# Kernel optimization log

Measured on AMD Instinct MI355X. Metric: run time of the kernel, lower is better.

The kernel has to match this reference:

```python
import jax, jax.numpy as jnp
import numpy as np

N, E = 50000, 800000
FN, FE, D, H = 64, 16, 128, 4


def setup_inputs() -> dict:
    key = jax.random.key(0)
    ks = jax.random.split(key, 16)
    inp = {
        "nodes": jax.random.normal(ks[0], (N, FN), jnp.float32),
        "edges": jax.random.normal(ks[1], (E, FE), jnp.float32),
        "senders": jax.random.randint(ks[2], (E,), 0, N, jnp.int32),
        "receivers": jax.random.randint(ks[3], (E,), 0, N, jnp.int32),
        "avg_multi_head": 0,
        # params (orthogonal init approximated by scaled normal; math identical)
        "W_node": jax.random.normal(ks[4], (FN, D), jnp.float32) / np.sqrt(FN),
        "b_node": jnp.zeros((D,), jnp.float32),
        "W_edge": jax.random.normal(ks[5], (FE, D), jnp.float32) / np.sqrt(FE),
        "b_edge": jnp.zeros((D,), jnp.float32),
        "Wk_s": jax.random.normal(ks[6], (H, D, D), jnp.float32) / np.sqrt(D),
        "bk_s": jnp.zeros((H, D), jnp.float32),
        "Wk_r": jax.random.normal(ks[7], (H, D, D), jnp.float32) / np.sqrt(D),
        "bk_r": jnp.zeros((H, D), jnp.float32),
        "W_out": jax.random.normal(ks[8], (H * D, D), jnp.float32) / np.sqrt(H * D),
        "b_out": jnp.zeros((D,), jnp.float32),
    }
    return inp


def _segment_softmax(logits, seg_ids, num_segments):
    seg_max = jax.ops.segment_max(logits, seg_ids, num_segments=num_segments)
    seg_max = jnp.where(jnp.isfinite(seg_max), seg_max, 0.0)  # empty segments
    e = jnp.exp(logits - seg_max[seg_ids])
    seg_sum = jax.ops.segment_sum(e, seg_ids, num_segments=num_segments)
    return e / seg_sum[seg_ids]


def reference(nodes, edges, senders, receivers, avg_multi_head,
              W_node, b_node, W_edge, b_edge, Wk_s, bk_s, Wk_r, bk_r,
              W_out, b_out):
    n_node = nodes.shape[0]
    x = nodes @ W_node + b_node            # [N, D] projected nodes
    ef = edges @ W_edge + b_edge           # [E, D] projected edge features
    sa = x[senders]                        # [E, D] sent attributes
    ra = x[receivers]                      # [E, D] received attributes
    scale = 1.0 / jnp.sqrt(jnp.asarray(D, x.dtype))
    heads = []
    for h in range(H):  # small fixed head count, structurally distinct params
        k_s = sa @ Wk_s[h] + bk_s[h]                 # [E, D]
        k_r = ra @ Wk_r[h] + bk_r[h] + ef            # [E, D]
        logits = jnp.sum(k_s * k_r, axis=1) * scale  # [E]
        w = _segment_softmax(logits, receivers, n_node)
        msg = w[:, None] * (sa + ef)                 # [E, D]
        heads.append(jax.ops.segment_sum(msg, receivers, num_segments=n_node))
    if avg_multi_head:
        agg = jnp.mean(jnp.stack(heads), axis=0)
    else:
        agg = jnp.concatenate(heads, axis=1) @ W_out + b_out
    return jax.nn.relu(x + agg)            # new node features [N, D]
```

## Files before the change

kernel.cpp:

```cpp
#include <hip/hip_runtime.h>

typedef unsigned short u16;
typedef unsigned int u32;
typedef short bh8 __attribute__((ext_vector_type(8)));
typedef float f4 __attribute__((ext_vector_type(4)));
typedef float pf2 __attribute__((ext_vector_type(2)));

__device__ __forceinline__ float bf2f(u16 h) { return __uint_as_float(((u32)h) << 16); }
__device__ __forceinline__ float bflo(u32 u) { return __uint_as_float(u << 16); }
__device__ __forceinline__ float bfhi(u32 u) { return __uint_as_float(u & 0xffff0000u); }
__device__ __forceinline__ u16 f2bf(float f) {
    u32 x = __float_as_uint(f);
    return (u16)((x + 0x7fffu + ((x >> 16) & 1u)) >> 16);
}
__device__ __forceinline__ pf2 pkfma(pf2 a, pf2 b, pf2 c) {
    pf2 d;
    asm("v_pk_fma_f32 %0, %1, %2, %3" : "=v"(d) : "v"(a), "v"(b), "v"(c));
    return d;
}
__device__ __forceinline__ pf2 u2f2(u32 u) {
    pf2 r;
    r.x = bflo(u);
    r.y = bfhi(u);
    return r;
}
__device__ __forceinline__ float dpp_red16(float x) {
    int y;
    y = __builtin_amdgcn_update_dpp(0, __float_as_int(x), 0xB1, 0xF, 0xF, true);
    x += __int_as_float(y);
    y = __builtin_amdgcn_update_dpp(0, __float_as_int(x), 0x4E, 0xF, 0xF, true);
    x += __int_as_float(y);
    y = __builtin_amdgcn_update_dpp(0, __float_as_int(x), 0x141, 0xF, 0xF, true);
    x += __int_as_float(y);
    y = __builtin_amdgcn_update_dpp(0, __float_as_int(x), 0x140, 0xF, 0xF, true);
    x += __int_as_float(y);
    return x;
}

#define KSCL 0.12751744336457488f

__global__ void k0a_kernel(const float* __restrict__ Wn, const float* __restrict__ Wks,
                           const float* __restrict__ Wkr, const float* __restrict__ Wout,
                           const float* __restrict__ bn, const float* __restrict__ bks,
                           const float* __restrict__ bkr, float* __restrict__ A,
                           float* __restrict__ B, u16* __restrict__ WoT,
                           float* __restrict__ ybs, float* __restrict__ ybr) {
    int idx = blockIdx.x * 256 + threadIdx.x;
    if (idx < 65536) {
        int which = idx >> 15;
        int rem = idx & 32767;
        int h = rem >> 13;
        int r = rem & 8191;
        int a = r >> 7, dp = r & 127;
        const float* W = which ? Wks : Wkr;
        float acc = 0.f;
        for (int d = 0; d < 128; ++d)
            acc += Wn[a * 128 + d] * W[(h * 128 + d) * 128 + dp];
        (which ? B : A)[(h * 64 + a) * 128 + dp] = acc;
    } else if (idx < 131072) {
        int j = idx - 65536;
        int c = j >> 9, k = j & 511;
        WoT[j] = f2bf(Wout[(size_t)k * 128 + c]);
    } else if (idx < 132096) {
        int j = idx - 131072;
        int which = j >> 9;
        int rem = j & 511;
        int h = rem >> 7, dp = rem & 127;
        const float* W = which ? Wks : Wkr;
        const float* b = which ? bks : bkr;
        float acc = b[h * 128 + dp];
        for (int d = 0; d < 128; ++d) acc += bn[d] * W[(h * 128 + d) * 128 + dp];
        (which ? ybs : ybr)[h * 128 + dp] = acc;
    }
}

__global__ void k0b_kernel(const float* __restrict__ Wn, const float* __restrict__ bn,
                           const float* __restrict__ A, const float* __restrict__ B,
                           const float* __restrict__ ybr, const float* __restrict__ ybs,
                           const float* __restrict__ Wks, const float* __restrict__ Wedge,
                           const float* __restrict__ bks, const float* __restrict__ bedge,
                           u16* __restrict__ WfT, float* __restrict__ biasrow) {
    int idx = blockIdx.x * 256 + threadIdx.x;
    if (idx >= 65 * 708 + 60 * 64) return;
    if (idx >= 65 * 708) {
        int j = idx - 65 * 708;
        WfT[(708 + (j >> 6)) * 64 + (j & 63)] = 0;
        return;
    }
    int a = idx / 708, c = idx % 708;
    float val;
    if (c < 128) {
        val = (a < 64) ? Wn[a * 128 + c] : bn[c];
    } else if (c < 640) {
        int h = (c - 128) >> 7, i = (c - 128) & 127;
        const float* rv = (a < 64) ? &A[(h * 64 + a) * 128] : &ybr[h * 128];
        float s = 0.f;
        for (int d = 0; d < 128; ++d) s += rv[d] * Wks[(h * 128 + i) * 128 + d];
        val = s;
    } else if (c < 704) {
        int k = (c - 640) >> 2, h = (c - 640) & 3;
        const float* rv = (a < 64) ? &B[(h * 64 + a) * 128] : &ybs[h * 128];
        float s = 0.f;
        for (int d = 0; d < 128; ++d) s += rv[d] * Wedge[k * 128 + d];
        val = s;
    } else {
        int h = c - 704;
        const float* rv = (a < 64) ? &B[(h * 64 + a) * 128] : &ybs[h * 128];
        float s = 0.f;
        for (int d = 0; d < 128; ++d) s += rv[d] * bedge[d];
        val = s;
    }
    if (a < 64) WfT[(size_t)c * 64 + a] = f2bf(val);
    else biasrow[c] = val;
}

__global__ __launch_bounds__(256) void g1_kernel(const float* __restrict__ nodes,
                                                 const u16* __restrict__ WfT,
                                                 const float* __restrict__ biasrow,
                                                 u16* __restrict__ Xc, u16* __restrict__ V,
                                                 u16* __restrict__ U, float* __restrict__ E0,
                                                 int N) {
    __shared__ u16 Asm[64][72];
    __shared__ u16 Bsm[128][72];
    int t = threadIdx.x;
    int r0 = blockIdx.x * 64, c0 = blockIdx.y * 128;
    {
        int row = t >> 2, cb = (t & 3) * 16;
        int r = r0 + row;
        u16 pk[16];
        if (r < N) {
            const float* src = &nodes[(size_t)r * 64 + cb];
#pragma unroll
            for (int q = 0; q < 16; ++q) pk[q] = f2bf(src[q]);
        } else {
#pragma unroll
            for (int q = 0; q < 16; ++q) pk[q] = 0;
        }
        *(uint4*)&Asm[row][cb] = *(const uint4*)&pk[0];
        *(uint4*)&Asm[row][cb + 8] = *(const uint4*)&pk[8];
    }
    {
        int col = t >> 1, ks = (t & 1) * 32;
        const u16* src = &WfT[(size_t)(c0 + col) * 64 + ks];
        uint4 v0 = *(const uint4*)src;
        uint4 v1 = *(const uint4*)(src + 8);
        uint4 v2 = *(const uint4*)(src + 16);
        uint4 v3 = *(const uint4*)(src + 24);
        *(uint4*)&Bsm[col][ks] = v0;
        *(uint4*)&Bsm[col][ks + 8] = v1;
        *(uint4*)&Bsm[col][ks + 16] = v2;
        *(uint4*)&Bsm[col][ks + 24] = v3;
    }
    __syncthreads();
    int lane = t & 63, wave = t >> 6;
    int wm = wave >> 1, wn = wave & 1;
    int lr = lane & 15, lk = lane >> 4;
    f4 acc[2][4] = {};
#pragma unroll
    for (int kk = 0; kk < 2; ++kk) {
        bh8 a[2], b[4];
#pragma unroll
        for (int am = 0; am < 2; ++am)
            a[am] = *(const bh8*)&Asm[wm * 32 + am * 16 + lr][kk * 32 + lk * 8];
#pragma unroll
        for (int bn = 0; bn < 4; ++bn)
            b[bn] = *(const bh8*)&Bsm[wn * 64 + bn * 16 + lr][kk * 32 + lk * 8];
#pragma unroll
        for (int am = 0; am < 2; ++am)
#pragma unroll
            for (int bn = 0; bn < 4; ++bn)
                acc[am][bn] = __builtin_amdgcn_mfma_f32_16x16x32_bf16(a[am], b[bn], acc[am][bn], 0, 0, 0);
    }
#pragma unroll
    for (int am = 0; am < 2; ++am)
#pragma unroll
        for (int bn = 0; bn < 4; ++bn) {
            int c = c0 + wn * 64 + bn * 16 + lr;
            if (c < 708) {
                float brow = biasrow[c];
#pragma unroll
                for (int q = 0; q < 4; ++q) {
                    int r = r0 + wm * 32 + am * 16 + lk * 4 + q;
                    if (r < N) {
                        float val = acc[am][bn][q] + brow;
                        if (c < 128) Xc[(size_t)r * 128 + c] = f2bf(val);
                        else if (c < 640) V[(size_t)r * 512 + (c - 128)] = f2bf(val * KSCL);
                        else if (c < 704) U[(size_t)r * 64 + (c - 640)] = f2bf(val * KSCL);
                        else E0[(size_t)r * 4 + (c - 704)] = exp2f(val * KSCL);
                    }
                }
            }
        }
}

__global__ void hist_kernel(const int* __restrict__ recv, int* __restrict__ deg, int E) {
    int e = blockIdx.x * 256 + threadIdx.x;
    if (e < E) atomicAdd(&deg[recv[e]], 1);
}

__global__ __launch_bounds__(1024) void scan1_kernel(const int* __restrict__ deg,
                                                     int* __restrict__ pre,
                                                     int* __restrict__ bsum, int N) {
    __shared__ int sm[1024];
    int b = blockIdx.x, t = threadIdx.x;
    int i = b * 1024 + t;
    int v = (i < N) ? deg[i] : 0;
    sm[t] = v;
    __syncthreads();
    for (int off = 1; off < 1024; off <<= 1) {
        int u = (t >= off) ? sm[t - off] : 0;
        __syncthreads();
        sm[t] += u;
        __syncthreads();
    }
    if (i < N) pre[i] = sm[t] - v;
    if (t == 1023) bsum[b] = sm[1023];
}

__global__ void scan2_kernel(int* __restrict__ bsum, int* __restrict__ boff, int nb) {
    int t = threadIdx.x;
    int own = (t < nb) ? bsum[t] : 0;
    int v = own;
#pragma unroll
    for (int off = 1; off < 64; off <<= 1) {
        int u = __shfl_up(v, off);
        if (t >= off) v += u;
    }
    if (t < nb) boff[t] = v - own;
    if (t == 63) boff[64] = v;
}

__global__ void scan3_kernel(const int* __restrict__ pre, const int* __restrict__ boff,
                             int* __restrict__ row_start, int* __restrict__ cursor, int N) {
    int i = blockIdx.x * 1024 + threadIdx.x;
    if (i < N) {
        int rsv = pre[i] + boff[i >> 10];
        row_start[i] = rsv;
        cursor[i] = rsv;
    }
    if (i == N) row_start[N] = boff[64];
}

__global__ void scatter_kernel(const int* __restrict__ recv, const int* __restrict__ senders,
                               int* __restrict__ cursor, int2* __restrict__ esp, int E) {
    int e = blockIdx.x * 256 + threadIdx.x;
    if (e < E) {
        int s = senders[e];
        int p = atomicAdd(&cursor[recv[e]], 1);
        esp[p] = make_int2(e, s);
    }
}

__global__ __launch_bounds__(256, 3) void en_kernel(const int* __restrict__ row_start,
                                                    const int2* __restrict__ esp,
                                                    const float* __restrict__ edges,
                                                    const u16* __restrict__ Xc,
                                                    const u16* __restrict__ V,
                                                    const u16* __restrict__ Uu,
                                                    const float* __restrict__ E0,
                                                    const float* __restrict__ W_edge,
                                                    const float* __restrict__ b_edge,
                                                    u16* __restrict__ agg, int N) {
    __shared__ float Wl[2048];
    int t = threadIdx.x;
    for (int i = t; i < 2048; i += 256) {
        int k = i >> 7, ch = i & 127;
        int pos = (k << 7) | ((((ch >> 1) & 3) << 5) | (((ch >> 3) & 15) << 1) | (ch & 1));
        Wl[pos] = W_edge[i];
    }
    __syncthreads();
    int lane = t & 63, wid = t >> 6;
    int g = lane >> 4, k16 = lane & 15;
    int nw = blockIdx.x * 4 + wid;
    int NW = gridDim.x * 4;

#define IDX8(ea, sa, eb, sb, s_)                                            \
    {                                                                       \
        int ev = 0, sv = 0;                                                 \
        if (lane < 8) {                                                     \
            int jj = (s_)*8 + lane;                                         \
            if (jj >= deg) jj = deg - 1;                                    \
            int2 pv = esp[rs + jj];                                         \
            ev = pv.x; sv = pv.y;                                           \
        }                                                                   \
        ea = __shfl(ev, g); sa = __shfl(sv, g);                             \
        eb = __shfl(ev, 4 + g); sb = __shfl(sv, 4 + g);                     \
    }

#define LOADP(Xq, Uq, Eq, Zq, eI, sI)                                       \
    {                                                                       \
        Xq = *(const uint4*)(Xc + (size_t)(sI)*128 + 8 * k16);              \
        Uq = *(const uint2*)(Uu + (size_t)(sI)*64 + k16 * 4);               \
        Eq = edges[(size_t)(eI)*16 + k16];                                  \
        Zq = *(const float4*)(E0 + (size_t)(sI)*4);                         \
    }

#define COMP(Xq, Uq, Eq, Zq, act)                                           \
    {                                                                       \
        pf2 X0 = u2f2(Xq.x), X1 = u2f2(Xq.y), X2 = u2f2(Xq.z), X3 = u2f2(Xq.w); \
        float uh[4] = {bflo(Uq.x), bfhi(Uq.x), bflo(Uq.y), bfhi(Uq.y)};     \
        float e0a[4] = {Zq.x, Zq.y, Zq.z, Zq.w};                            \
        _Pragma("unroll") for (int h = 0; h < 4; ++h) {                     \
            pf2 p2 = {Eq * uh[h], 0.f};                                     \
            p2 = pkfma(X0, vr[h][0], p2); p2 = pkfma(X1, vr[h][1], p2);     \
            p2 = pkfma(X2, vr[h][2], p2); p2 = pkfma(X3, vr[h][3], p2);     \
            float p = dpp_red16(p2.x + p2.y);                               \
            float wh = (act) ? e0a[h] * exp2f(p) : 0.f;                     \
            Ss[h] += wh; aE[h] = fmaf(wh, Eq, aE[h]);                       \
            pf2 w2 = {wh, wh};                                              \
            aX[h][0] = pkfma(w2, X0, aX[h][0]);                             \
            aX[h][1] = pkfma(w2, X1, aX[h][1]);                             \
            aX[h][2] = pkfma(w2, X2, aX[h][2]);                             \
            aX[h][3] = pkfma(w2, X3, aX[h][3]);                             \
        }                                                                   \
    }

    int n = nw;
    if (n >= N) return;
    int rs = row_start[n];
    int re = row_start[n + 1];
    while (true) {
        int deg = re - rs;
        int n2 = n + NW;
        bool more = (n2 < N);
        int rs2 = rs, re2 = re;
        if (more) {
            rs2 = row_start[n2];
            re2 = row_start[n2 + 1];
        }
        const u16* Vr = V + (size_t)n * 512;
        pf2 vr[4][4];
#pragma unroll
        for (int h = 0; h < 4; ++h) {
            uint4 v = *(const uint4*)(Vr + h * 128 + 8 * k16);
            vr[h][0] = u2f2(v.x); vr[h][1] = u2f2(v.y);
            vr[h][2] = u2f2(v.z); vr[h][3] = u2f2(v.w);
        }
        pf2 aX[4][4] = {};
        float Ss[4] = {0.f, 0.f, 0.f, 0.f};
        float aE[4] = {0.f, 0.f, 0.f, 0.f};

        if (deg > 0) {
            int nst = (deg + 7) >> 3;
            int eA0, sA0, eA1, sA1, eB0, sB0, eB1, sB1;
            IDX8(eA0, sA0, eA1, sA1, 0);
            uint4 xP0, xP1; uint2 uP0, uP1; float eP0, eP1; float4 zP0, zP1;
            LOADP(xP0, uP0, eP0, zP0, eA0, sA0);
            LOADP(xP1, uP1, eP1, zP1, eA1, sA1);
            if (nst > 1) {
                IDX8(eB0, sB0, eB1, sB1, 1);
            } else {
                eB0 = eA0; sB0 = sA0; eB1 = eA1; sB1 = sA1;
            }
            for (int s = 0; s < nst; ++s) {
                uint4 xc0 = xP0, xc1 = xP1;
                uint2 uc0 = uP0, uc1 = uP1;
                float ec0 = eP0, ec1 = eP1;
                float4 zc0 = zP0, zc1 = zP1;
                int base = s * 8;
                if (s + 1 < nst) {
                    LOADP(xP0, uP0, eP0, zP0, eB0, sB0);
                    LOADP(xP1, uP1, eP1, zP1, eB1, sB1);
                    if (s + 2 < nst) IDX8(eB0, sB0, eB1, sB1, s + 2);
                }
                COMP(xc0, uc0, ec0, zc0, base + g < deg);
                COMP(xc1, uc1, ec1, zc1, base + 4 + g < deg);
            }
        }
#pragma unroll
        for (int h = 0; h < 4; ++h) {
#pragma unroll
            for (int i = 0; i < 4; ++i) {
                pf2 v = aX[h][i];
                v.x += __shfl_xor(v.x, 16); v.y += __shfl_xor(v.y, 16);
                v.x += __shfl_xor(v.x, 32); v.y += __shfl_xor(v.y, 32);
                aX[h][i] = v;
            }
            Ss[h] += __shfl_xor(Ss[h], 16); Ss[h] += __shfl_xor(Ss[h], 32);
            aE[h] += __shfl_xor(aE[h], 16); aE[h] += __shfl_xor(aE[h], 32);
        }
        pf2 axg[4];
#pragma unroll
        for (int i = 0; i < 4; ++i)
            axg[i] = g == 0 ? aX[0][i] : g == 1 ? aX[1][i] : g == 2 ? aX[2][i] : aX[3][i];
        float aEg = g == 0 ? aE[0] : g == 1 ? aE[1] : g == 2 ? aE[2] : aE[3];
        float Sg = g == 0 ? Ss[0] : g == 1 ? Ss[1] : g == 2 ? Ss[2] : Ss[3];
        const pf2* Wp = (const pf2*)Wl;
#pragma unroll
        for (int kk = 0; kk < 16; ++kk) {
            float a = __shfl(aEg, (g << 4) | kk);
            pf2 a2 = {a, a};
            int base = (kk << 6) + k16;
            axg[0] = pkfma(a2, Wp[base], axg[0]);
            axg[1] = pkfma(a2, Wp[base + 16], axg[1]);
            axg[2] = pkfma(a2, Wp[base + 32], axg[2]);
            axg[3] = pkfma(a2, Wp[base + 48], axg[3]);
        }
        {
            float inv = (deg > 0 && Sg > 0.f) ? 1.f / Sg : 0.f;
            float bes = (deg > 0) ? 1.f : 0.f;
            const float* br = &b_edge[8 * k16];
            u32 o0 = (u32)f2bf(axg[0].x * inv + bes * br[0]) |
                     ((u32)f2bf(axg[0].y * inv + bes * br[1]) << 16);
            u32 o1 = (u32)f2bf(axg[1].x * inv + bes * br[2]) |
                     ((u32)f2bf(axg[1].y * inv + bes * br[3]) << 16);
            u32 o2 = (u32)f2bf(axg[2].x * inv + bes * br[4]) |
                     ((u32)f2bf(axg[2].y * inv + bes * br[5]) << 16);
            u32 o3 = (u32)f2bf(axg[3].x * inv + bes * br[6]) |
                     ((u32)f2bf(axg[3].y * inv + bes * br[7]) << 16);
            uint4 st = {o0, o1, o2, o3};
            *(uint4*)(agg + (size_t)n * 512 + g * 128 + 8 * k16) = st;
        }
        if (!more) break;
        n = n2; rs = rs2; re = re2;
    }
#undef IDX8
#undef LOADP
#undef COMP
}

__global__ __launch_bounds__(256) void g3_kernel(const u16* __restrict__ Xc,
                                                 const u16* __restrict__ agg,
                                                 const u16* __restrict__ WoT,
                                                 const float* __restrict__ bout,
                                                 const int* __restrict__ avgflag,
                                                 float* __restrict__ out, int N) {
    int t = threadIdx.x;
    int r0 = blockIdx.x * 64;
    if (*avgflag) {
        for (int i = t; i < 64 * 128; i += 256) {
            int n = r0 + (i >> 7), j = i & 127;
            if (n < N) {
                float s = 0.f;
#pragma unroll
                for (int h = 0; h < 4; ++h) s += bf2f(agg[(size_t)n * 512 + h * 128 + j]);
                float v = bf2f(Xc[(size_t)n * 128 + j]) + 0.25f * s;
                out[(size_t)n * 128 + j] = v > 0.f ? v : 0.f;
            }
        }
        return;
    }
    __shared__ u16 Asm[64][72];
    __shared__ u16 Bsm[128][72];
    int lane = t & 63, wave = t >> 6;
    int wm = wave >> 1, wn = wave & 1;
    int lr = lane & 15, lk = lane >> 4;
    f4 acc[2][4] = {};
    for (int kb = 0; kb < 8; ++kb) {
        if (kb) __syncthreads();
        {
            int row = t >> 2, ks = (t & 3) * 16;
            int r = r0 + row;
            uint4 v0 = {0, 0, 0, 0}, v1 = {0, 0, 0, 0};
            if (r < N) {
                const u16* src = &agg[(size_t)r * 512 + kb * 64 + ks];
                v0 = *(const uint4*)src;
                v1 = *(const uint4*)(src + 8);
            }
            *(uint4*)&Asm[row][ks] = v0;
            *(uint4*)&Asm[row][ks + 8] = v1;
        }
        {
            int col = t >> 1, ks = (t & 1) * 32;
            const u16* src = &WoT[(size_t)col * 512 + kb * 64 + ks];
            uint4 v0 = *(const uint4*)src;
            uint4 v1 = *(const uint4*)(src + 8);
            uint4 v2 = *(const uint4*)(src + 16);
            uint4 v3 = *(const uint4*)(src + 24);
            *(uint4*)&Bsm[col][ks] = v0;
            *(uint4*)&Bsm[col][ks + 8] = v1;
            *(uint4*)&Bsm[col][ks + 16] = v2;
            *(uint4*)&Bsm[col][ks + 24] = v3;
        }
        __syncthreads();
#pragma unroll
        for (int kk = 0; kk < 2; ++kk) {
            bh8 a[2], b[4];
#pragma unroll
            for (int am = 0; am < 2; ++am)
                a[am] = *(const bh8*)&Asm[wm * 32 + am * 16 + lr][kk * 32 + lk * 8];
#pragma unroll
            for (int bn = 0; bn < 4; ++bn)
                b[bn] = *(const bh8*)&Bsm[wn * 64 + bn * 16 + lr][kk * 32 + lk * 8];
#pragma unroll
            for (int am = 0; am < 2; ++am)
#pragma unroll
                for (int bn = 0; bn < 4; ++bn)
                    acc[am][bn] = __builtin_amdgcn_mfma_f32_16x16x32_bf16(a[am], b[bn], acc[am][bn], 0, 0, 0);
        }
    }
#pragma unroll
    for (int am = 0; am < 2; ++am)
#pragma unroll
        for (int bn = 0; bn < 4; ++bn) {
            int c = wn * 64 + bn * 16 + lr;
            float bc = bout[c];
#pragma unroll
            for (int q = 0; q < 4; ++q) {
                int r = r0 + wm * 32 + am * 16 + lk * 4 + q;
                if (r < N) {
                    float v = acc[am][bn][q] + bc + bf2f(Xc[(size_t)r * 128 + c]);
                    out[(size_t)r * 128 + c] = v > 0.f ? v : 0.f;
                }
            }
        }
}

extern "C" void kernel_launch(void* const* d_in, const int* in_sizes, int n_in, void* d_out,
                              int out_size, void* d_ws, size_t ws_size, hipStream_t stream) {
    const float* nodes = (const float*)d_in[0];
    const float* edges = (const float*)d_in[1];
    const int* senders = (const int*)d_in[2];
    const int* receivers = (const int*)d_in[3];
    const int* avgflag = (const int*)d_in[4];
    const float* W_node = (const float*)d_in[5];
    const float* b_node = (const float*)d_in[6];
    const float* W_edge = (const float*)d_in[7];
    const float* b_edge = (const float*)d_in[8];
    const float* Wk_s = (const float*)d_in[9];
    const float* bk_s = (const float*)d_in[10];
    const float* Wk_r = (const float*)d_in[11];
    const float* bk_r = (const float*)d_in[12];
    const float* W_out = (const float*)d_in[13];
    const float* b_out = (const float*)d_in[14];
    int N = in_sizes[0] / 64;
    int E = in_sizes[2];
    float* outp = (float*)d_out;

    char* base = (char*)d_ws;
    size_t off = 0;
    auto alloc = [&](size_t nbytes) -> char* {
        char* p = base + off;
        off = (off + nbytes + 255) & ~(size_t)255;
        return p;
    };
    u16* Xc = (u16*)alloc((size_t)N * 128 * 2);
    u16* V = (u16*)alloc((size_t)N * 512 * 2);
    u16* U = (u16*)alloc((size_t)N * 64 * 2);
    float* E0 = (float*)alloc((size_t)N * 4 * 4);
    u16* agg = (u16*)alloc((size_t)N * 512 * 2);
    int* deg = (int*)alloc((size_t)N * 4);
    int* row_start = (int*)alloc((size_t)(N + 1) * 4);
    int* cursor = (int*)alloc((size_t)N * 4);
    int2* esp = (int2*)alloc((size_t)E * 8);
    int* pre = (int*)alloc((size_t)N * 4);
    int* bsum = (int*)alloc((size_t)128 * 4);
    int* boff = (int*)alloc((size_t)128 * 4);
    float* A = (float*)alloc((size_t)4 * 64 * 128 * 4);
    float* B = (float*)alloc((size_t)4 * 64 * 128 * 4);
    float* ybr = (float*)alloc((size_t)4 * 128 * 4);
    float* ybs = (float*)alloc((size_t)4 * 128 * 4);
    float* biasrow = (float*)alloc((size_t)712 * 4);
    u16* WfT = (u16*)alloc((size_t)768 * 64 * 2);
    u16* WoT = (u16*)alloc((size_t)128 * 512 * 2);

    int nb = (N + 1023) >> 10;

    hipMemsetAsync(deg, 0, (size_t)N * 4, stream);
    k0a_kernel<<<(132096 + 255) / 256, 256, 0, stream>>>(W_node, Wk_s, Wk_r, W_out, b_node,
                                                         bk_s, bk_r, A, B, WoT, ybs, ybr);
    k0b_kernel<<<(65 * 708 + 60 * 64 + 255) / 256, 256, 0, stream>>>(
        W_node, b_node, A, B, ybr, ybs, Wk_s, W_edge, bk_s, b_edge, WfT, biasrow);
    dim3 g1grid((N + 63) / 64, 6);
    g1_kernel<<<g1grid, 256, 0, stream>>>(nodes, WfT, biasrow, Xc, V, U, E0, N);
    hist_kernel<<<(E + 255) / 256, 256, 0, stream>>>(receivers, deg, E);
    scan1_kernel<<<nb, 1024, 0, stream>>>(deg, pre, bsum, N);
    scan2_kernel<<<1, 64, 0, stream>>>(bsum, boff, nb);
    scan3_kernel<<<(N + 1024) / 1024, 1024, 0, stream>>>(pre, boff, row_start, cursor, N);
    scatter_kernel<<<(E + 255) / 256, 256, 0, stream>>>(receivers, senders, cursor, esp, E);
    en_kernel<<<4096, 256, 0, stream>>>(row_start, esp, edges, Xc, V, U, E0, W_edge,
                                        b_edge, agg, N);
    g3_kernel<<<(N + 63) / 64, 256, 0, stream>>>(Xc, agg, WoT, b_out, avgflag, outp, N);
}
```

Baseline: 325.8 us.

## Permute edge features into CSR order as bf16 during scatter

The scatter kernel now converts each edge's 16 float features to bf16 and writes them at the edge's CSR position. It also stores sender ids in a separate int array instead of (edge, sender) pairs. The edge-node kernel then reads edge features contiguously by CSR slot rather than gathering them randomly by original edge id, and it no longer shuffles edge ids. This trades an extra permuted write in scatter, plus reduced precision on edge features, for coalesced, smaller reads in the main aggregation loop.

```diff
diff --git a/kernel.cpp b/kernel.cpp
--- a/kernel.cpp
+++ b/kernel.cpp
@@ -242,18 +242,26 @@
 }
 
 __global__ void scatter_kernel(const int* __restrict__ recv, const int* __restrict__ senders,
-                               int* __restrict__ cursor, int2* __restrict__ esp, int E) {
+                               const float* __restrict__ edges, int* __restrict__ cursor,
+                               int* __restrict__ s_csr, u16* __restrict__ eperm, int E) {
     int e = blockIdx.x * 256 + threadIdx.x;
     if (e < E) {
         int s = senders[e];
+        const float* src = &edges[(size_t)e * 16];
+        u16 tmp[16];
+#pragma unroll
+        for (int k = 0; k < 16; ++k) tmp[k] = f2bf(src[k]);
         int p = atomicAdd(&cursor[recv[e]], 1);
-        esp[p] = make_int2(e, s);
+        s_csr[p] = s;
+        u16* dst = &eperm[(size_t)p * 16];
+        *(uint4*)dst = *(const uint4*)&tmp[0];
+        *(uint4*)(dst + 8) = *(const uint4*)&tmp[8];
     }
 }
 
 __global__ __launch_bounds__(256, 3) void en_kernel(const int* __restrict__ row_start,
-                                                    const int2* __restrict__ esp,
-                                                    const float* __restrict__ edges,
+                                                    const int* __restrict__ s_csr,
+                                                    const u16* __restrict__ eperm,
                                                     const u16* __restrict__ Xc,
                                                     const u16* __restrict__ V,
                                                     const u16* __restrict__ Uu,
@@ -274,25 +282,29 @@
     int nw = blockIdx.x * 4 + wid;
     int NW = gridDim.x * 4;
 
-#define IDX8(ea, sa, eb, sb, s_)                                            \
+#define IDXS(sa, sb, s_)                                                    \
     {                                                                       \
-        int ev = 0, sv = 0;                                                 \
+        int sv = 0;                                                         \
         if (lane < 8) {                                                     \
             int jj = (s_)*8 + lane;                                         \
             if (jj >= deg) jj = deg - 1;                                    \
-            int2 pv = esp[rs + jj];                                         \
-            ev = pv.x; sv = pv.y;                                           \
+            sv = s_csr[rs + jj];                                            \
         }                                                                   \
-        ea = __shfl(ev, g); sa = __shfl(sv, g);                             \
-        eb = __shfl(ev, 4 + g); sb = __shfl(sv, 4 + g);                     \
-    }
-
-#define LOADP(Xq, Uq, Eq, Zq, eI, sI)                                       \
+        sa = __shfl(sv, g); sb = __shfl(sv, 4 + g);                         \
+    }
+
+#define LOADP(Xq, Uq, Zq, sI)                                               \
     {                                                                       \
         Xq = *(const uint4*)(Xc + (size_t)(sI)*128 + 8 * k16);              \
         Uq = *(const uint2*)(Uu + (size_t)(sI)*64 + k16 * 4);               \
-        Eq = edges[(size_t)(eI)*16 + k16];                                  \
         Zq = *(const float4*)(E0 + (size_t)(sI)*4);                         \
+    }
+
+#define ELOAD(Eq, slot)                                                     \
+    {                                                                       \
+        int _j = (slot);                                                    \
+        if (_j > deg - 1) _j = deg - 1;                                     \
+        Eq = bf2f(eperm[(size_t)(rs + _j) * 16 + k16]);                     \
     }
 
 #define COMP(Xq, Uq, Eq, Zq, act)                                           \
@@ -342,15 +354,17 @@
 
         if (deg > 0) {
             int nst = (deg + 7) >> 3;
-            int eA0, sA0, eA1, sA1, eB0, sB0, eB1, sB1;
-            IDX8(eA0, sA0, eA1, sA1, 0);
-            uint4 xP0, xP1; uint2 uP0, uP1; float eP0, eP1; float4 zP0, zP1;
-            LOADP(xP0, uP0, eP0, zP0, eA0, sA0);
-            LOADP(xP1, uP1, eP1, zP1, eA1, sA1);
+            int sA0, sA1, sB0, sB1;
+            IDXS(sA0, sA1, 0);
+            uint4 xP0, xP1; uint2 uP0, uP1; float4 zP0, zP1; float eP0, eP1;
+            LOADP(xP0, uP0, zP0, sA0);
+            LOADP(xP1, uP1, zP1, sA1);
+            ELOAD(eP0, g);
+            ELOAD(eP1, 4 + g);
             if (nst > 1) {
-                IDX8(eB0, sB0, eB1, sB1, 1);
+                IDXS(sB0, sB1, 1);
             } else {
-                eB0 = eA0; sB0 = sA0; eB1 = eA1; sB1 = sA1;
+                sB0 = sA0; sB1 = sA1;
             }
             for (int s = 0; s < nst; ++s) {
                 uint4 xc0 = xP0, xc1 = xP1;
@@ -359,9 +373,11 @@
                 float4 zc0 = zP0, zc1 = zP1;
                 int base = s * 8;
                 if (s + 1 < nst) {
-                    LOADP(xP0, uP0, eP0, zP0, eB0, sB0);
-                    LOADP(xP1, uP1, eP1, zP1, eB1, sB1);
-                    if (s + 2 < nst) IDX8(eB0, sB0, eB1, sB1, s + 2);
+                    LOADP(xP0, uP0, zP0, sB0);
+                    LOADP(xP1, uP1, zP1, sB1);
+                    ELOAD(eP0, base + 8 + g);
+                    ELOAD(eP1, base + 12 + g);
+                    if (s + 2 < nst) IDXS(sB0, sB1, s + 2);
                 }
                 COMP(xc0, uc0, ec0, zc0, base + g < deg);
                 COMP(xc1, uc1, ec1, zc1, base + 4 + g < deg);
@@ -414,8 +430,9 @@
         if (!more) break;
         n = n2; rs = rs2; re = re2;
     }
-#undef IDX8
+#undef IDXS
 #undef LOADP
+#undef ELOAD
 #undef COMP
 }
 
@@ -542,7 +559,8 @@
     int* deg = (int*)alloc((size_t)N * 4);
     int* row_start = (int*)alloc((size_t)(N + 1) * 4);
     int* cursor = (int*)alloc((size_t)N * 4);
-    int2* esp = (int2*)alloc((size_t)E * 8);
+    int* s_csr = (int*)alloc((size_t)E * 4);
+    u16* eperm = (u16*)alloc((size_t)E * 16 * 2);
     int* pre = (int*)alloc((size_t)N * 4);
     int* bsum = (int*)alloc((size_t)128 * 4);
     int* boff = (int*)alloc((size_t)128 * 4);
@@ -567,8 +585,9 @@
     scan1_kernel<<<nb, 1024, 0, stream>>>(deg, pre, bsum, N);
     scan2_kernel<<<1, 64, 0, stream>>>(bsum, boff, nb);
     scan3_kernel<<<(N + 1024) / 1024, 1024, 0, stream>>>(pre, boff, row_start, cursor, N);
-    scatter_kernel<<<(E + 255) / 256, 256, 0, stream>>>(receivers, senders, cursor, esp, E);
-    en_kernel<<<4096, 256, 0, stream>>>(row_start, esp, edges, Xc, V, U, E0, W_edge,
+    scatter_kernel<<<(E + 255) / 256, 256, 0, stream>>>(receivers, senders, edges, cursor,
+                                                        s_csr, eperm, E);
+    en_kernel<<<4096, 256, 0, stream>>>(row_start, s_csr, eperm, Xc, V, U, E0, W_edge,
                                         b_edge, agg, N);
     g3_kernel<<<(N + 63) / 64, 256, 0, stream>>>(Xc, agg, WoT, b_out, avgflag, outp, N);
 }
```

Measured after the change: 320.2 us. About the same (-1.7%).
